# Performance work log

Measured on AMD Instinct MI355X. Metric: run time of the kernel, lower is better.

## Reference

```python
import jax, jax.numpy as jnp
import numpy as np

# constants from __init__ defaults
K_WINNERS = 5
GAIN_UP = 1.8
MIN_GAIN = 0.5
MAX_GAIN = 2.5
THETA = 1.0

B, T = 512, 8192


def setup_inputs() -> dict:
    key = jax.random.key(0)
    k1, k2, k3 = jax.random.split(key, 3)
    amp = jax.random.uniform(k1, (B, T), jnp.float32)
    pitch = jax.random.uniform(k2, (B, T), jnp.float32)
    boundary = jax.random.uniform(k3, (B, T), jnp.float32)
    decay = jnp.array([0.7, 0.7, 0.7], jnp.float32)    # buffer 'decay'
    weights = jnp.array([1.0, 1.0, 1.0], jnp.float32)  # buffer 'weights'
    return {"amp": amp, "pitch": pitch, "boundary": boundary,
            "decay": decay, "weights": weights}


def reference(amp, pitch, boundary, decay, weights):
    # Stack the 3 channels so one scan handles all LIF neurons: xs [3, B, T]
    xs = jnp.stack([amp, pitch, boundary], axis=0)
    d = decay[:, None]  # [3, 1] broadcast over batch

    def step(v, x_t):          # v, x_t: [3, B]
        v = d * v + x_t
        s = (v >= THETA).astype(v.dtype)
        return v - s * THETA, s

    v0 = jnp.zeros((3, B), xs.dtype)
    _, spikes = jax.lax.scan(step, v0, jnp.moveaxis(xs, 2, 0))  # spikes [T, 3, B]

    # salience = w_amp*s_amp + w_pitch*s_pitch + w_bound*s_bound -> [B, T]
    sal = jnp.einsum('c,tcb->bt', weights, spikes)
    # smoothing == 0 -> conv branch skipped (matches default init)
    sal = sal / (jnp.max(sal, axis=1, keepdims=True) + 1e-6)

    topk_vals, topk_idx = jax.lax.top_k(sal, K_WINNERS)  # [B, K]
    avg_winner = topk_vals.mean(axis=1)                  # [B]
    mu_scalar = MIN_GAIN + (MAX_GAIN - MIN_GAIN) * jnp.tanh(GAIN_UP * avg_winner)
    return mu_scalar, sal, topk_idx
```

## Files before the change

kernel.cpp:

```cpp
#include <hip/hip_runtime.h>
#include <cstdint>
#include <cstddef>

#define BB 512
#define TT 8192
#define TW 256
#define KWIN 5

static __device__ __forceinline__ float fract_f(float x) {
#if __has_builtin(__builtin_amdgcn_fractf)
    return __builtin_amdgcn_fractf(x);
#else
    return x - floorf(x);
#endif
}

__global__ __launch_bounds__(64, 2)
void lif_scan_kernel(const float* __restrict__ amp,
                     const float* __restrict__ pitch,
                     const float* __restrict__ boundary,
                     const float* __restrict__ decay,
                     float* __restrict__ out)
{
    const int blk = blockIdx.x;
    const int c   = blk >> 9;
    const int b   = blk & 511;
    const int l   = threadIdx.x;
    const float* __restrict__ src =
        (c == 0 ? amp : (c == 1 ? pitch : boundary)) + (size_t)b * TT;
    const float dv = decay[c];

    const float4* s4 = reinterpret_cast<const float4*>(src);
    float4 kr[32];
#pragma unroll
    for (int j = 0; j < 32; ++j)
        kr[j] = s4[32 * l + j];

    float v = 0.0f;
    const bool z = (l == 0);

    {
        auto shuf4 = [](float4 a) {
            float4 r;
            r.x = __shfl_up(a.x, 1, 64);
            r.y = __shfl_up(a.y, 1, 64);
            r.z = __shfl_up(a.z, 1, 64);
            r.w = __shfl_up(a.w, 1, 64);
            return r;
        };
        float4 W0, W1;
        W0 = shuf4(kr[0]);
#define WSTEP(xx)                                               \
        {                                                       \
            float x = (xx);                                     \
            if (z) x = 0.0f;                                    \
            float t2 = __fadd_rn(__fmul_rn(dv, v), x);          \
            v = fract_f(t2);                                    \
        }
#pragma unroll
        for (int j = 0; j < 32; j += 2) {
            W1 = shuf4(kr[j + 1]);
            WSTEP(W0.x) WSTEP(W0.y) WSTEP(W0.z) WSTEP(W0.w)
            if (j + 2 < 32) W0 = shuf4(kr[j + 2]);
            WSTEP(W1.x) WSTEP(W1.y) WSTEP(W1.z) WSTEP(W1.w)
        }
#undef WSTEP
    }

    uint32_t w[4];
    {
        float bs;
#define KSTEP(xx)                                               \
        {                                                       \
            float t2 = __fadd_rn(__fmul_rn(dv, v), (xx));       \
            float nv = fract_f(t2);                             \
            bs = __builtin_fmaf(2.0f, bs, t2 - nv);             \
            v = nv;                                             \
        }
#pragma unroll
        for (int q = 0; q < 4; ++q) {
            bs = 0.0f;
#pragma unroll
            for (int i = 0; i < 4; ++i) {
                const float4 a = kr[8 * q + i];
                KSTEP(a.x) KSTEP(a.y) KSTEP(a.z) KSTEP(a.w)
            }
            const uint32_t hi = (uint32_t)bs;
            bs = 0.0f;
#pragma unroll
            for (int i = 0; i < 4; ++i) {
                const float4 a = kr[8 * q + 4 + i];
                KSTEP(a.x) KSTEP(a.y) KSTEP(a.z) KSTEP(a.w)
            }
            w[q] = (hi << 16) | (uint32_t)bs;
        }
#undef KSTEP
    }

    uint32_t* wout = reinterpret_cast<uint32_t*>(out + 512 + (size_t)b * TT)
                   + c * TW;
    *reinterpret_cast<uint4*>(wout + 4 * l) = make_uint4(w[0], w[1], w[2], w[3]);
}

__global__ __launch_bounds__(256, 2)
void salience_topk_kernel(const float* __restrict__ weights,
                          float* __restrict__ out)
{
    const int b = blockIdx.x;
    const int tid = threadIdx.x;

    __shared__ uint32_t words[3 * TW];
    __shared__ uint32_t spres[4];
    __shared__ float ntab[8];
    __shared__ uint32_t htab[8];
    __shared__ unsigned long long red[4];
    __shared__ unsigned long long wins;

    float* sal_out = out + 512 + (size_t)b * TT;
    const uint32_t* wsrc = reinterpret_cast<const uint32_t*>(sal_out);

    words[tid]       = wsrc[tid];
    words[tid + 256] = wsrc[tid + 256];
    words[tid + 512] = wsrc[tid + 512];

    const float w0 = weights[0], w1 = weights[1], w2 = weights[2];
    __syncthreads();

    uint32_t pres = 0;
#pragma unroll
    for (int j = 0; j < 8; ++j) {
        const int t0 = 4 * tid + 1024 * j;
        const int wi = t0 >> 5;
        const uint32_t wa = words[wi], wp = words[TW + wi], wq = words[2 * TW + wi];
#pragma unroll
        for (int k = 0; k < 4; ++k) {
            const int sh = 31 - ((t0 & 31) + k);
            const uint32_t idx = ((wa >> sh) & 1u)
                               | (((wp >> sh) & 1u) << 1)
                               | (((wq >> sh) & 1u) << 2);
            pres |= (1u << idx);
        }
    }
#pragma unroll
    for (int off = 32; off; off >>= 1)
        pres |= __shfl_down(pres, off);
    if ((tid & 63) == 0) spres[tid >> 6] = pres;
    __syncthreads();

    if (tid < 8) {
        const uint32_t p = spres[0] | spres[1] | spres[2] | spres[3];
        float s0 = (float)(tid & 1), s1 = (float)((tid >> 1) & 1), s2 = (float)(tid >> 2);
        float tv = __fadd_rn(__fadd_rn(__fmul_rn(w0, s0), __fmul_rn(w1, s1)),
                             __fmul_rn(w2, s2));
        float m = ((p >> tid) & 1u) ? tv : -INFINITY;
        m = fmaxf(m, __shfl_xor(m, 1));
        m = fmaxf(m, __shfl_xor(m, 2));
        m = fmaxf(m, __shfl_xor(m, 4));
        const float denom = __fadd_rn(m, 1e-6f);
        float nv = tv / denom;
        ntab[tid] = nv;
        uint32_t ub = __float_as_uint(nv);
        htab[tid] = (ub & 0x80000000u) ? ~ub : (ub | 0x80000000u);
    }
    __syncthreads();

    unsigned long long t5[5] = {0ull, 0ull, 0ull, 0ull, 0ull};
#pragma unroll
    for (int j = 0; j < 8; ++j) {
        const int t0 = 4 * tid + 1024 * j;
        const int wi = t0 >> 5;
        const uint32_t wa = words[wi], wp = words[TW + wi], wq = words[2 * TW + wi];
        float4 q;
        float* qp = &q.x;
#pragma unroll
        for (int k = 0; k < 4; ++k) {
            const int sh = 31 - ((t0 & 31) + k);
            const uint32_t idx = ((wa >> sh) & 1u)
                               | (((wp >> sh) & 1u) << 1)
                               | (((wq >> sh) & 1u) << 2);
            qp[k] = ntab[idx];
            unsigned long long key = ((unsigned long long)htab[idx] << 32)
                                   | (unsigned long long)(uint32_t)(TT - 1 - (t0 + k));
            if (key > t5[4]) {
#pragma unroll
                for (int i = 0; i < 5; ++i) {
                    bool g = key > t5[i];
                    unsigned long long o = t5[i];
                    t5[i] = g ? key : o;
                    key   = g ? o : key;
                }
            }
        }
        *reinterpret_cast<float4*>(sal_out + t0) = q;
    }

    float vsum = 0.0f;
    for (int r = 0; r < KWIN; ++r) {
        unsigned long long cand = t5[0];
#pragma unroll
        for (int off = 32; off; off >>= 1) {
            unsigned long long o = __shfl_down(cand, off);
            if (o > cand) cand = o;
        }
        __syncthreads();
        if ((tid & 63) == 0) red[tid >> 6] = cand;
        __syncthreads();
        if (tid == 0) {
            unsigned long long m = red[0];
            if (red[1] > m) m = red[1];
            if (red[2] > m) m = red[2];
            if (red[3] > m) m = red[3];
            wins = m;
        }
        __syncthreads();
        const unsigned long long w = wins;
        if (t5[0] == w) {
            t5[0] = t5[1]; t5[1] = t5[2]; t5[2] = t5[3]; t5[3] = t5[4]; t5[4] = 0ull;
        }
        if (tid == 0) {
            uint32_t hi = (uint32_t)(w >> 32);
            uint32_t fb = (hi & 0x80000000u) ? (hi & 0x7FFFFFFFu) : ~hi;
            vsum += __uint_as_float(fb);
            out[512 + (size_t)BB * TT + (size_t)b * KWIN + r] =
                (float)(int)(TT - 1 - (uint32_t)(w & 0xFFFFFFFFull));
        }
    }

    if (tid == 0) {
        out[b] = 0.5f + 2.0f * tanhf(1.8f * (vsum / 5.0f));
    }
}

extern "C" void kernel_launch(void* const* d_in, const int* in_sizes, int n_in,
                              void* d_out, int out_size, void* d_ws, size_t ws_size,
                              hipStream_t stream) {
    const float* amp      = (const float*)d_in[0];
    const float* pitch    = (const float*)d_in[1];
    const float* boundary = (const float*)d_in[2];
    const float* decay    = (const float*)d_in[3];
    const float* weights  = (const float*)d_in[4];
    float* out = (float*)d_out;

    lif_scan_kernel<<<3 * BB, 64, 0, stream>>>(amp, pitch, boundary, decay, out);
    salience_topk_kernel<<<BB, 256, 0, stream>>>(weights, out);
}
```

Baseline: 111.9 us.

## Fuse LIF scan and salience/top-k into one kernel via shared memory

Merges the per-channel LIF scan kernel and the salience/top-k kernel into a single block per batch row. Three waves each scan one channel and write packed spike bitwords into shared memory instead of global scratch, then all four waves do the salience and top-k. This removes a kernel launch and a global-memory round trip of the bitwords. In exchange, one wave sits idle during the scan, and scheduling now happens at block granularity rather than per channel wave.

```diff
diff --git a/kernel.cpp b/kernel.cpp
--- a/kernel.cpp
+++ b/kernel.cpp
@@ -15,116 +15,105 @@
 #endif
 }
 
-__global__ __launch_bounds__(64, 2)
-void lif_scan_kernel(const float* __restrict__ amp,
-                     const float* __restrict__ pitch,
-                     const float* __restrict__ boundary,
-                     const float* __restrict__ decay,
-                     float* __restrict__ out)
+__global__ __launch_bounds__(256, 2)
+void fused_lif_salience_kernel(const float* __restrict__ amp,
+                               const float* __restrict__ pitch,
+                               const float* __restrict__ boundary,
+                               const float* __restrict__ decay,
+                               const float* __restrict__ weights,
+                               float* __restrict__ out)
 {
-    const int blk = blockIdx.x;
-    const int c   = blk >> 9;
-    const int b   = blk & 511;
-    const int l   = threadIdx.x;
-    const float* __restrict__ src =
-        (c == 0 ? amp : (c == 1 ? pitch : boundary)) + (size_t)b * TT;
-    const float dv = decay[c];
-
-    const float4* s4 = reinterpret_cast<const float4*>(src);
-    float4 kr[32];
-#pragma unroll
-    for (int j = 0; j < 32; ++j)
-        kr[j] = s4[32 * l + j];
-
-    float v = 0.0f;
-    const bool z = (l == 0);
-
-    {
-        auto shuf4 = [](float4 a) {
-            float4 r;
-            r.x = __shfl_up(a.x, 1, 64);
-            r.y = __shfl_up(a.y, 1, 64);
-            r.z = __shfl_up(a.z, 1, 64);
-            r.w = __shfl_up(a.w, 1, 64);
-            return r;
-        };
-        float4 W0, W1;
-        W0 = shuf4(kr[0]);
-#define WSTEP(xx)                                               \
-        {                                                       \
-            float x = (xx);                                     \
-            if (z) x = 0.0f;                                    \
-            float t2 = __fadd_rn(__fmul_rn(dv, v), x);          \
-            v = fract_f(t2);                                    \
-        }
-#pragma unroll
-        for (int j = 0; j < 32; j += 2) {
-            W1 = shuf4(kr[j + 1]);
-            WSTEP(W0.x) WSTEP(W0.y) WSTEP(W0.z) WSTEP(W0.w)
-            if (j + 2 < 32) W0 = shuf4(kr[j + 2]);
-            WSTEP(W1.x) WSTEP(W1.y) WSTEP(W1.z) WSTEP(W1.w)
-        }
-#undef WSTEP
-    }
-
-    uint32_t w[4];
-    {
-        float bs;
-#define KSTEP(xx)                                               \
-        {                                                       \
-            float t2 = __fadd_rn(__fmul_rn(dv, v), (xx));       \
-            float nv = fract_f(t2);                             \
-            bs = __builtin_fmaf(2.0f, bs, t2 - nv);             \
-            v = nv;                                             \
-        }
-#pragma unroll
-        for (int q = 0; q < 4; ++q) {
-            bs = 0.0f;
-#pragma unroll
-            for (int i = 0; i < 4; ++i) {
-                const float4 a = kr[8 * q + i];
-                KSTEP(a.x) KSTEP(a.y) KSTEP(a.z) KSTEP(a.w)
-            }
-            const uint32_t hi = (uint32_t)bs;
-            bs = 0.0f;
-#pragma unroll
-            for (int i = 0; i < 4; ++i) {
-                const float4 a = kr[8 * q + 4 + i];
-                KSTEP(a.x) KSTEP(a.y) KSTEP(a.z) KSTEP(a.w)
-            }
-            w[q] = (hi << 16) | (uint32_t)bs;
-        }
-#undef KSTEP
-    }
-
-    uint32_t* wout = reinterpret_cast<uint32_t*>(out + 512 + (size_t)b * TT)
-                   + c * TW;
-    *reinterpret_cast<uint4*>(wout + 4 * l) = make_uint4(w[0], w[1], w[2], w[3]);
-}
-
-__global__ __launch_bounds__(256, 2)
-void salience_topk_kernel(const float* __restrict__ weights,
-                          float* __restrict__ out)
-{
-    const int b = blockIdx.x;
+    const int b   = blockIdx.x;
     const int tid = threadIdx.x;
-
-    __shared__ uint32_t words[3 * TW];
+    const int wv  = tid >> 6;
+    const int l   = tid & 63;
+
+    __shared__ __align__(16) uint32_t words[3 * TW];
     __shared__ uint32_t spres[4];
     __shared__ float ntab[8];
     __shared__ uint32_t htab[8];
     __shared__ unsigned long long red[4];
     __shared__ unsigned long long wins;
 
+    if (wv < 3) {
+        const float* __restrict__ src =
+            (wv == 0 ? amp : (wv == 1 ? pitch : boundary)) + (size_t)b * TT;
+        const float dv = decay[wv];
+
+        const float4* s4 = reinterpret_cast<const float4*>(src);
+        float4 kr[32];
+#pragma unroll
+        for (int j = 0; j < 32; ++j)
+            kr[j] = s4[32 * l + j];
+
+        float v = 0.0f;
+        const bool z = (l == 0);
+
+        {
+            auto shuf4 = [](float4 a) {
+                float4 r;
+                r.x = __shfl_up(a.x, 1, 64);
+                r.y = __shfl_up(a.y, 1, 64);
+                r.z = __shfl_up(a.z, 1, 64);
+                r.w = __shfl_up(a.w, 1, 64);
+                return r;
+            };
+            float4 W0, W1;
+            W0 = shuf4(kr[0]);
+#define WSTEP(xx)                                               \
+            {                                                   \
+                float x = (xx);                                 \
+                if (z) x = 0.0f;                                \
+                float t2 = __fadd_rn(__fmul_rn(dv, v), x);      \
+                v = fract_f(t2);                                \
+            }
+#pragma unroll
+            for (int j = 0; j < 32; j += 2) {
+                W1 = shuf4(kr[j + 1]);
+                WSTEP(W0.x) WSTEP(W0.y) WSTEP(W0.z) WSTEP(W0.w)
+                if (j + 2 < 32) W0 = shuf4(kr[j + 2]);
+                WSTEP(W1.x) WSTEP(W1.y) WSTEP(W1.z) WSTEP(W1.w)
+            }
+#undef WSTEP
+        }
+
+        uint32_t w[4];
+        {
+            float bs;
+#define KSTEP(xx)                                               \
+            {                                                   \
+                float t2 = __fadd_rn(__fmul_rn(dv, v), (xx));   \
+                float nv = fract_f(t2);                         \
+                bs = __builtin_fmaf(2.0f, bs, t2 - nv);         \
+                v = nv;                                         \
+            }
+#pragma unroll
+            for (int q = 0; q < 4; ++q) {
+                bs = 0.0f;
+#pragma unroll
+                for (int i = 0; i < 4; ++i) {
+                    const float4 a = kr[8 * q + i];
+                    KSTEP(a.x) KSTEP(a.y) KSTEP(a.z) KSTEP(a.w)
+                }
+                const uint32_t hi = (uint32_t)bs;
+                bs = 0.0f;
+#pragma unroll
+                for (int i = 0; i < 4; ++i) {
+                    const float4 a = kr[8 * q + 4 + i];
+                    KSTEP(a.x) KSTEP(a.y) KSTEP(a.z) KSTEP(a.w)
+                }
+                w[q] = (hi << 16) | (uint32_t)bs;
+            }
+#undef KSTEP
+        }
+
+        *reinterpret_cast<uint4*>(&words[wv * TW + 4 * l]) =
+            make_uint4(w[0], w[1], w[2], w[3]);
+    }
+    __syncthreads();
+
     float* sal_out = out + 512 + (size_t)b * TT;
-    const uint32_t* wsrc = reinterpret_cast<const uint32_t*>(sal_out);
-
-    words[tid]       = wsrc[tid];
-    words[tid + 256] = wsrc[tid + 256];
-    words[tid + 512] = wsrc[tid + 512];
-
     const float w0 = weights[0], w1 = weights[1], w2 = weights[2];
-    __syncthreads();
 
     uint32_t pres = 0;
 #pragma unroll
@@ -241,6 +230,6 @@
     const float* weights  = (const float*)d_in[4];
     float* out = (float*)d_out;
 
-    lif_scan_kernel<<<3 * BB, 64, 0, stream>>>(amp, pitch, boundary, decay, out);
-    salience_topk_kernel<<<BB, 256, 0, stream>>>(weights, out);
+    fused_lif_salience_kernel<<<BB, 256, 0, stream>>>(amp, pitch, boundary,
+                                                      decay, weights, out);
 }
```

Measured after the change: 110.8 us. No clear change (-1.0%).
